# Kernel optimization log

Hardware: AMD Instinct MI355X
Metric: run time of the kernel (lower is better)

Reference implementation:

```python
import jax, jax.numpy as jnp
import numpy as np

NUM_HEADS = 8
IN_CH = 512
SCALING = float(IN_CH // 8) ** (-0.5)  # 0.125, as in the torch module


def _conv1x1(x, w, b):
    # x: [B,C,H,W], w: [O,C], b: [O]  (1x1 conv == channel matmul)
    return jnp.einsum('bchw,oc->bohw', x, w) + b[None, :, None, None]


def setup_inputs() -> dict:
    key = jax.random.key(0)
    ks = jax.random.split(key, 9)
    B, C, H, W = 4, IN_CH, 96, 96
    q = jax.random.normal(ks[0], (B, C, H, W), jnp.float32)
    v = jax.random.normal(ks[1], (B, C, H, W), jnp.float32)
    # xavier_uniform for [C,C] 1x1 conv weights
    limit = float(np.sqrt(6.0 / (C + C)))
    Wq = jax.random.uniform(ks[2], (C, C), jnp.float32, -limit, limit)
    Wk = jax.random.uniform(ks[3], (C, C), jnp.float32, -limit, limit)
    Wv = jax.random.uniform(ks[4], (C, C), jnp.float32, -limit, limit)
    bq = jnp.zeros((C,), jnp.float32)
    bk = jnp.zeros((C,), jnp.float32)
    bv = jnp.zeros((C,), jnp.float32)
    # gamma is init to 0 in the module; use a nonzero value so the output is nontrivial
    gamma = jax.random.normal(ks[5], (1,), jnp.float32) * 0.1
    return {'q': q, 'v': v, 'Wq': Wq, 'bq': bq, 'Wk': Wk, 'bk': bk,
            'Wv': Wv, 'bv': bv, 'gamma': gamma}


def reference(q, v, Wq, bq, Wk, bk, Wv, bv, gamma):
    B, C, H, W = q.shape
    nh = NUM_HEADS
    hd = C // nh
    t = _conv1x1(q, Wq, bq) * SCALING           # proj_query
    f = _conv1x1(q, Wk, bk)                     # proj_key
    g = _conv1x1(v, Wv, bv)                     # proj_value
    t = t.reshape(B * nh, hd, H, W)
    f = f.reshape(B * nh, hd, H, W)
    g = g.reshape(B * nh, hd, H, W)
    # criss-cross affinity: row (same y, all x') and column (same x, all y'!=y)
    e_row = jnp.einsum('bdyx,bdyi->byxi', t, f)  # [Bh, H, W, W]
    e_col = jnp.einsum('bdyx,bdix->byxi', t, f)  # [Bh, H, W, H]
    # exclude the current position from the column branch (CUDA kernel skips i==y)
    diag = (jnp.arange(H)[:, None, None] == jnp.arange(H)[None, None, :])  # [H,1,H]
    e_col = jnp.where(diag, -jnp.inf, e_col)
    attn = jax.nn.softmax(jnp.concatenate([e_row, e_col], axis=-1), axis=-1)  # [Bh,H,W,W+H]
    a_row, a_col = attn[..., :W], attn[..., W:]
    out = (jnp.einsum('byxi,bdyi->bdyx', a_row, g)
           + jnp.einsum('byxi,bdix->bdyx', a_col, g))  # [Bh, hd, H, W]
    out = out.reshape(B, C, H, W)
    return gamma[0] * out + v
```

## Files before the change

### kernel.cpp

```cpp
#include <hip/hip_runtime.h>
#include <hip/hip_bf16.h>

typedef __bf16 bf16;
typedef __attribute__((ext_vector_type(8))) __bf16 bf16x8;
typedef __attribute__((ext_vector_type(4))) float floatx4;

#define B_  4
#define C_  512
#define H_  96
#define W_  96
#define HD_ 64
#define HW_ 9216
#define BH_ 32
#define SCALING_ 0.125f
#define BHS_ 589824

static constexpr size_t T_ELEMS = (size_t)BH_ * HD_ * HW_;
static constexpr size_t S_ELEMS = (size_t)BH_ * HW_;

__global__ __launch_bounds__(256) void cast_w(
    const float* __restrict__ Wq, const float* __restrict__ Wk, const float* __restrict__ Wv,
    bf16* __restrict__ Wb)
{
    const int i  = blockIdx.x * 256 + threadIdx.x;
    const int e0 = i * 4;
    const int arr = e0 >> 18;
    const int off = e0 & 262143;
    const float* W = (arr == 0) ? Wq : (arr == 1) ? Wk : Wv;
    const float4 val = *(const float4*)(W + off);
    bf16 tmp[4] __attribute__((aligned(8)));
    tmp[0] = (bf16)val.x; tmp[1] = (bf16)val.y; tmp[2] = (bf16)val.z; tmp[3] = (bf16)val.w;
    *(uint2*)(Wb + e0) = *(const uint2*)tmp;
}

__global__ __launch_bounds__(256) void cast_qv(
    const float* __restrict__ q, const float* __restrict__ v,
    bf16* __restrict__ qbT, bf16* __restrict__ vbT)
{
    const int z = blockIdx.z;
    const int s = z >> 2, b = z & 3;
    const float* sb = (s ? v : q) + (size_t)b * C_ * HW_;
    bf16*       db = (s ? vbT : qbT) + (size_t)b * HW_ * C_;
    const int p0 = blockIdx.x * 64, c0 = blockIdx.y * 64;

    __shared__ float ts[64][65];
    const int tid = threadIdx.x;

    for (int i = tid; i < 1024; i += 256) {
        const int row = i >> 4, seg = i & 15;
        const float4 val = *(const float4*)(sb + (size_t)(c0 + row) * HW_ + p0 + seg * 4);
        ts[row][seg * 4 + 0] = val.x; ts[row][seg * 4 + 1] = val.y;
        ts[row][seg * 4 + 2] = val.z; ts[row][seg * 4 + 3] = val.w;
    }
    __syncthreads();
    for (int i = tid; i < 512; i += 256) {
        const int prow = i >> 3, cseg = i & 7;
        bf16 tmp[8] __attribute__((aligned(16)));
        #pragma unroll
        for (int k = 0; k < 8; k++) tmp[k] = (bf16)ts[cseg * 8 + k][prow];
        *(uint4*)(db + (size_t)(p0 + prow) * C_ + c0 + cseg * 8) = *(const uint4*)tmp;
    }
}

__device__ __forceinline__ void stage_swz(
    const bf16* __restrict__ A, const bf16* __restrict__ Bsrc,
    int o0, int p0, int k0, int tid, bf16* As, bf16* Bs)
{
    #pragma unroll
    for (int c = tid; c < 512; c += 256) {
        const int sc = c ^ ((c >> 3) & 7);
        const int row = sc >> 2, seg = sc & 3;
        const bf16* gA = A    + (size_t)(o0 + row) * C_ + k0 + seg * 8;
        const bf16* gB = Bsrc + (size_t)(p0 + row) * C_ + k0 + seg * 8;
#if __has_builtin(__builtin_amdgcn_global_load_lds)
        char* lA = (char*)As + (size_t)(c & ~63) * 16;
        char* lB = (char*)Bs + (size_t)(c & ~63) * 16;
        __builtin_amdgcn_global_load_lds((const __attribute__((address_space(1))) void*)gA,
                                         (__attribute__((address_space(3))) void*)lA, 16, 0, 0);
        __builtin_amdgcn_global_load_lds((const __attribute__((address_space(1))) void*)gB,
                                         (__attribute__((address_space(3))) void*)lB, 16, 0, 0);
#else
        *(uint4*)((char*)As + (size_t)c * 16) = *(const uint4*)gA;
        *(uint4*)((char*)Bs + (size_t)c * 16) = *(const uint4*)gB;
#endif
    }
}

__device__ __forceinline__ int swz_chunk(int r, int quad)
{
    return (r * 4 + quad) ^ ((r >> 1) & 7);
}

__device__ __forceinline__ void compute_swz(
    const bf16* As, const bf16* Bs,
    int mrow, int ncol, int l16, int quad, floatx4 acc[4][4])
{
    bf16x8 af[4], bf_[4];
    #pragma unroll
    for (int i = 0; i < 4; i++)
        af[i] = *(const bf16x8*)&As[swz_chunk(mrow + i * 16 + l16, quad) * 8];
    #pragma unroll
    for (int j = 0; j < 4; j++)
        bf_[j] = *(const bf16x8*)&Bs[swz_chunk(ncol + j * 16 + l16, quad) * 8];
    #pragma unroll
    for (int i = 0; i < 4; i++)
        #pragma unroll
        for (int j = 0; j < 4; j++)
            acc[i][j] = __builtin_amdgcn_mfma_f32_16x16x32_bf16(af[i], bf_[j], acc[i][j], 0, 0, 0);
}

__global__ __launch_bounds__(256) void conv_mfma(
    const bf16* __restrict__ Wb,
    const float* __restrict__ bq, const float* __restrict__ bk, const float* __restrict__ bv,
    const bf16* __restrict__ qbT, const bf16* __restrict__ vbT,
    bf16* __restrict__ tR, bf16* __restrict__ fR, bf16* __restrict__ g)
{
    const int z = blockIdx.z, arr = z >> 2, b = z & 3;
    const bf16* A    = Wb + (size_t)arr * C_ * C_;
    const bf16* Bsrc = ((arr == 2) ? vbT : qbT) + (size_t)b * HW_ * C_;
    const float* bias = (arr == 0) ? bq : (arr == 1) ? bk : bv;
    const float scale = (arr == 0) ? SCALING_ : 1.0f;

    const int p0 = blockIdx.x * 128;
    const int o0 = blockIdx.y * 128;

    __shared__ __align__(16) bf16 smem[17408];
    bf16* const As0 = smem;
    bf16* const Bs0 = smem + 4096;
    bf16* const As1 = smem + 8192;
    bf16* const Bs1 = smem + 12288;

    const int tid = threadIdx.x, lane = tid & 63;
    const int wave = tid >> 6, l16 = lane & 15, quad = lane >> 4;
    const int mrow = (wave >> 1) * 64, ncol = (wave & 1) * 64;

    floatx4 acc[4][4] = {};

    stage_swz(A, Bsrc, o0, p0, 0, tid, As0, Bs0);
    __syncthreads();

    for (int k0 = 0; k0 < C_; k0 += 64) {
        if (k0 + 32 < C_) stage_swz(A, Bsrc, o0, p0, k0 + 32, tid, As1, Bs1);
        compute_swz(As0, Bs0, mrow, ncol, l16, quad, acc);
        __syncthreads();
        if (k0 + 64 < C_) stage_swz(A, Bsrc, o0, p0, k0 + 64, tid, As0, Bs0);
        compute_swz(As1, Bs1, mrow, ncol, l16, quad, acc);
        __syncthreads();
    }

    if (arr < 2) {
        #pragma unroll
        for (int i = 0; i < 4; i++)
            #pragma unroll
            for (int r = 0; r < 4; r++) {
                const int ol_ = mrow + i * 16 + quad * 4 + r;
                const float bi = bias[o0 + ol_];
                #pragma unroll
                for (int j = 0; j < 4; j++) {
                    const int pl = ncol + j * 16 + l16;
                    smem[pl * 128 + (ol_ ^ ((pl & 7) << 3))] = (bf16)((acc[i][j][r] + bi) * scale);
                }
            }
        __syncthreads();
        bf16* dst = (arr == 0) ? tR : fR;
        #pragma unroll
        for (int c = tid; c < 2048; c += 256) {
            const int pl = c >> 4, oo = c & 15;
            const int pg = p0 + pl;
            const int y = pg / 96, x = pg - y * 96;
            const int og = o0 + oo * 8;
            const int bh = b * 8 + (og >> 6), d = og & 63;
            const size_t di = (size_t)bh * BHS_ + (size_t)y * 6144 + x * 64 + d;
            *(uint4*)(dst + di) = *(const uint4*)&smem[pl * 128 + ((oo ^ (pl & 7)) * 8)];
        }
    } else {
        const int TS = 136;
        #pragma unroll
        for (int i = 0; i < 4; i++)
            #pragma unroll
            for (int r = 0; r < 4; r++) {
                const int ol_ = mrow + i * 16 + quad * 4 + r;
                const float bi = bias[o0 + ol_];
                #pragma unroll
                for (int j = 0; j < 4; j++) {
                    const int pl = ncol + j * 16 + l16;
                    smem[ol_ * TS + pl] = (bf16)(acc[i][j][r] + bi);
                }
            }
        __syncthreads();
        #pragma unroll
        for (int c = tid; c < 2048; c += 256) {
            const int ol_ = c >> 4, po = c & 15;
            const size_t di = (size_t)(b * 512 + o0 + ol_) * HW_ + p0 + po * 8;
            *(uint4*)(g + di) = *(const uint4*)&smem[ol_ * TS + po * 8];
        }
    }
}

__global__ __launch_bounds__(256) void transpose_g(const bf16* __restrict__ src, bf16* __restrict__ dst)
{
    const int plane = blockIdx.y;
    const int y0 = blockIdx.x * 32;
    const bf16* s = src + (size_t)plane * HW_;
    bf16*       d = dst + (size_t)plane * HW_;

    __shared__ bf16 ts[32][100];
    const int tid = threadIdx.x;

    #pragma unroll
    for (int i = tid; i < 768; i += 256) {
        const int row = i / 24, seg = i % 24;
        *(uint2*)&ts[row][seg * 4] = *(const uint2*)(s + (size_t)(y0 + row) * W_ + seg * 4);
    }
    __syncthreads();
    #pragma unroll
    for (int i = tid; i < 768; i += 256) {
        const int x = i >> 3, yseg = i & 7;
        bf16 tmp[4] __attribute__((aligned(8)));
        #pragma unroll
        for (int k = 0; k < 4; k++) tmp[k] = ts[yseg * 4 + k][x];
        *(uint2*)(d + (size_t)x * H_ + y0 + yseg * 4) = *(const uint2*)tmp;
    }
}

__global__ __launch_bounds__(512) void attn_col(
    const bf16* __restrict__ tR, const bf16* __restrict__ fR, const bf16* __restrict__ gT,
    bf16* __restrict__ outC, float* __restrict__ mc, float* __restrict__ lc)
{
    const int x = blockIdx.x;
    const int bh = blockIdx.y;

    __shared__ __align__(16) bf16 tl[96][72];
    __shared__ __align__(16) bf16 fl[96][72];
    __shared__ __align__(16) bf16 el[96][104];

    const int tid = threadIdx.x;
    const size_t sbase = (size_t)bh * BHS_;

    for (int i = tid; i < 768; i += 512) {
        const int y = i >> 3, oct = i & 7;
        const size_t gi = sbase + (size_t)y * 6144 + (size_t)x * 64 + oct * 8;
        *(uint4*)&tl[y][oct * 8] = *(const uint4*)(tR + gi);
        *(uint4*)&fl[y][oct * 8] = *(const uint4*)(fR + gi);
    }
    __syncthreads();

    const int lane = tid & 63, wave = tid >> 6;
    const int l16 = lane & 15, quad = lane >> 4;

    __builtin_amdgcn_s_setprio(1);
    #pragma unroll
    for (int it = 0; it < 5; it++) {
        const int idx = wave + it * 8;
        if (idx < 36) {
            const int mt = idx / 6, nt = idx % 6;
            floatx4 a = {};
            #pragma unroll
            for (int ks = 0; ks < 2; ks++) {
                bf16x8 af = *(const bf16x8*)&tl[mt * 16 + l16][ks * 32 + quad * 8];
                bf16x8 bf_ = *(const bf16x8*)&fl[nt * 16 + l16][ks * 32 + quad * 8];
                a = __builtin_amdgcn_mfma_f32_16x16x32_bf16(af, bf_, a, 0, 0, 0);
            }
            #pragma unroll
            for (int r = 0; r < 4; r++) {
                const int row = mt * 16 + quad * 4 + r, col = nt * 16 + l16;
                el[row][col] = (row == col) ? (bf16)(-1e30f) : (bf16)a[r];
            }
        }
    }
    __builtin_amdgcn_s_setprio(0);
    __syncthreads();

    bf16 (*gl)[104] = (bf16 (*)[104])fl;
    const size_t gbase = sbase + (size_t)x * 96;
    for (int i = tid; i < 768; i += 512) {
        const int d = i / 12, seg = i % 12;
        *(uint4*)&gl[d][seg * 8] = *(const uint4*)(gT + gbase + (size_t)d * HW_ + seg * 8);
    }

    if (tid < 384) {
        const int r = tid >> 2, qu = tid & 3;
        float vals[24];
        float m = -1e30f;
        #pragma unroll
        for (int k = 0; k < 3; k++) {
            bf16x8 v8 = *(const bf16x8*)&el[r][qu * 24 + k * 8];
            #pragma unroll
            for (int e = 0; e < 8; e++) { vals[k * 8 + e] = (float)v8[e]; m = fmaxf(m, vals[k * 8 + e]); }
        }
        m = fmaxf(m, __shfl_xor(m, 1));
        m = fmaxf(m, __shfl_xor(m, 2));
        float s = 0.f;
        #pragma unroll
        for (int k = 0; k < 3; k++) {
            bf16 tmp[8] __attribute__((aligned(16)));
            #pragma unroll
            for (int e = 0; e < 8; e++) {
                const float p = __expf(vals[k * 8 + e] - m);
                s += p; tmp[e] = (bf16)p;
            }
            *(uint4*)&el[r][qu * 24 + k * 8] = *(const uint4*)tmp;
        }
        s += __shfl_xor(s, 1);
        s += __shfl_xor(s, 2);
        if (qu == 0) {
            mc[(size_t)bh * HW_ + x * 96 + r] = m;
            lc[(size_t)bh * HW_ + x * 96 + r] = s;
        }
    }
    __syncthreads();

    bf16 (*ol)[72] = tl;
    __builtin_amdgcn_s_setprio(1);
    #pragma unroll
    for (int it = 0; it < 3; it++) {
        const int idx = wave + it * 8;
        const int mt = idx >> 2, nt = idx & 3;
        floatx4 a = {};
        #pragma unroll
        for (int ks = 0; ks < 3; ks++) {
            bf16x8 pf = *(const bf16x8*)&el[mt * 16 + l16][ks * 32 + quad * 8];
            bf16x8 gf = *(const bf16x8*)&gl[nt * 16 + l16][ks * 32 + quad * 8];
            a = __builtin_amdgcn_mfma_f32_16x16x32_bf16(pf, gf, a, 0, 0, 0);
        }
        #pragma unroll
        for (int r = 0; r < 4; r++)
            ol[mt * 16 + quad * 4 + r][nt * 16 + l16] = (bf16)a[r];
    }
    __builtin_amdgcn_s_setprio(0);
    __syncthreads();

    bf16* ob = outC + sbase + (size_t)x * 6144;
    for (int i = tid; i < 768; i += 512) {
        const int j = i >> 3, oct = i & 7;
        *(uint4*)(ob + (size_t)j * 64 + oct * 8) = *(const uint4*)&ol[j][oct * 8];
    }
}

__global__ __launch_bounds__(512) void attn_row_merge(
    const bf16* __restrict__ tR, const bf16* __restrict__ fR, const bf16* __restrict__ g,
    const bf16* __restrict__ outC, const float* __restrict__ mc, const float* __restrict__ lc,
    const float* __restrict__ v, const float* __restrict__ gamma, float* __restrict__ out)
{
    const int y = blockIdx.x;
    const int bh = blockIdx.y;

    __shared__ __align__(16) bf16 tl[96][72];
    __shared__ __align__(16) bf16 fl[96][72];
    __shared__ __align__(16) bf16 el[96][104];
    __shared__ float mll[96], lll[96], wrl[96], wcl[96];

    const int tid = threadIdx.x;
    const size_t sbase = (size_t)bh * BHS_;
    const size_t slice = sbase + (size_t)y * 6144;

    for (int i = tid; i < 768; i += 512) {
        const int j = i >> 3, oct = i & 7;
        *(uint4*)&tl[j][oct * 8] = *(const uint4*)(tR + slice + (size_t)j * 64 + oct * 8);
        *(uint4*)&fl[j][oct * 8] = *(const uint4*)(fR + slice + (size_t)j * 64 + oct * 8);
    }

    uint4 oc0, oc1 = {};
    {
        const int xx = tid >> 3, oct = tid & 7;
        oc0 = *(const uint4*)(outC + sbase + (size_t)xx * 6144 + (size_t)y * 64 + oct * 8);
    }
    if (tid < 256) {
        const int i1 = tid + 512, xx = i1 >> 3, oct = i1 & 7;
        oc1 = *(const uint4*)(outC + sbase + (size_t)xx * 6144 + (size_t)y * 64 + oct * 8);
    }
    float4 vp0a, vp0b, vp1a = {}, vp1b = {};
    {
        const int xo = tid >> 6, d = tid & 63;
        const size_t ob = sbase + (size_t)d * HW_ + (size_t)y * 96 + xo * 8;
        vp0a = *(const float4*)(v + ob);
        vp0b = *(const float4*)(v + ob + 4);
    }
    if (tid < 256) {
        const int i1 = tid + 512, xo = i1 >> 6, d = i1 & 63;
        const size_t ob = sbase + (size_t)d * HW_ + (size_t)y * 96 + xo * 8;
        vp1a = *(const float4*)(v + ob);
        vp1b = *(const float4*)(v + ob + 4);
    }
    float mcv = 0.f, lcv = 0.f;
    if (tid < 96) {
        mcv = mc[(size_t)bh * HW_ + tid * 96 + y];
        lcv = lc[(size_t)bh * HW_ + tid * 96 + y];
    }
    __syncthreads();

    const int lane = tid & 63, wave = tid >> 6;
    const int l16 = lane & 15, quad = lane >> 4;

    __builtin_amdgcn_s_setprio(1);
    #pragma unroll
    for (int it = 0; it < 5; it++) {
        const int idx = wave + it * 8;
        if (idx < 36) {
            const int mt = idx / 6, nt = idx % 6;
            floatx4 a = {};
            #pragma unroll
            for (int ks = 0; ks < 2; ks++) {
                bf16x8 af = *(const bf16x8*)&tl[mt * 16 + l16][ks * 32 + quad * 8];
                bf16x8 bf_ = *(const bf16x8*)&fl[nt * 16 + l16][ks * 32 + quad * 8];
                a = __builtin_amdgcn_mfma_f32_16x16x32_bf16(af, bf_, a, 0, 0, 0);
            }
            #pragma unroll
            for (int r = 0; r < 4; r++)
                el[mt * 16 + quad * 4 + r][nt * 16 + l16] = (bf16)a[r];
        }
    }
    __builtin_amdgcn_s_setprio(0);
    __syncthreads();

    bf16 (*gl)[104] = (bf16 (*)[104])tl;
    const size_t gbase = sbase + (size_t)y * 96;
    for (int i = tid; i < 768; i += 512) {
        const int d = i / 12, seg = i % 12;
        *(uint4*)&gl[d][seg * 8] = *(const uint4*)(g + gbase + (size_t)d * HW_ + seg * 8);
    }

    bf16 (*ocl)[72] = fl;
    {
        const int xx = tid >> 3, oct = tid & 7;
        *(uint4*)&ocl[xx][oct * 8] = oc0;
    }
    if (tid < 256) {
        const int i1 = tid + 512, xx = i1 >> 3, oct = i1 & 7;
        *(uint4*)&ocl[xx][oct * 8] = oc1;
    }

    if (tid < 384) {
        const int r = tid >> 2, qu = tid & 3;
        float vals[24];
        float m = -1e30f;
        #pragma unroll
        for (int k = 0; k < 3; k++) {
            bf16x8 v8 = *(const bf16x8*)&el[r][qu * 24 + k * 8];
            #pragma unroll
            for (int e = 0; e < 8; e++) { vals[k * 8 + e] = (float)v8[e]; m = fmaxf(m, vals[k * 8 + e]); }
        }
        m = fmaxf(m, __shfl_xor(m, 1));
        m = fmaxf(m, __shfl_xor(m, 2));
        float s = 0.f;
        #pragma unroll
        for (int k = 0; k < 3; k++) {
            bf16 tmp[8] __attribute__((aligned(16)));
            #pragma unroll
            for (int e = 0; e < 8; e++) {
                const float p = __expf(vals[k * 8 + e] - m);
                s += p; tmp[e] = (bf16)p;
            }
            *(uint4*)&el[r][qu * 24 + k * 8] = *(const uint4*)tmp;
        }
        s += __shfl_xor(s, 1);
        s += __shfl_xor(s, 2);
        if (qu == 0) { mll[r] = m; lll[r] = s; }
    }
    __syncthreads();

    if (tid < 96) {
        const float mrv = mll[tid], lrv = lll[tid];
        const float mm = fmaxf(mrv, mcv);
        const float wr = __expf(mrv - mm), wc = __expf(mcv - mm);
        const float dn = lrv * wr + lcv * wc;
        wrl[tid] = wr / dn;
        wcl[tid] = wc / dn;
    }
    floatx4 pa[3] = {};
    __builtin_amdgcn_s_setprio(1);
    #pragma unroll
    for (int it = 0; it < 3; it++) {
        const int idx = wave + it * 8;
        const int mt = idx >> 2, nt = idx & 3;
        #pragma unroll
        for (int ks = 0; ks < 3; ks++) {
            bf16x8 pf = *(const bf16x8*)&el[mt * 16 + l16][ks * 32 + quad * 8];
            bf16x8 gf = *(const bf16x8*)&gl[nt * 16 + l16][ks * 32 + quad * 8];
            pa[it] = __builtin_amdgcn_mfma_f32_16x16x32_bf16(pf, gf, pa[it], 0, 0, 0);
        }
    }
    __builtin_amdgcn_s_setprio(0);
    __syncthreads();

    #pragma unroll
    for (int it = 0; it < 3; it++) {
        const int idx = wave + it * 8;
        const int mt = idx >> 2, nt = idx & 3;
        #pragma unroll
        for (int r = 0; r < 4; r++)
            el[mt * 16 + quad * 4 + r][nt * 16 + l16] = (bf16)pa[it][r];
    }
    __syncthreads();

    const float gam = gamma[0];
    {
        const int xo = tid >> 6, d = tid & 63;
        const int x0 = xo * 8;
        float res[8];
        #pragma unroll
        for (int k = 0; k < 8; k++) {
            const int xx = x0 + k;
            res[k] = (float)el[xx][d] * wrl[xx] + (float)ocl[xx][d] * wcl[xx];
        }
        const size_t ob = sbase + (size_t)d * HW_ + (size_t)y * 96 + x0;
        float4 r0, r1;
        r0.x = gam * res[0] + vp0a.x; r0.y = gam * res[1] + vp0a.y;
        r0.z = gam * res[2] + vp0a.z; r0.w = gam * res[3] + vp0a.w;
        r1.x = gam * res[4] + vp0b.x; r1.y = gam * res[5] + vp0b.y;
        r1.z = gam * res[6] + vp0b.z; r1.w = gam * res[7] + vp0b.w;
        *(float4*)(out + ob) = r0;
        *(float4*)(out + ob + 4) = r1;
    }
    if (tid < 256) {
        const int i1 = tid + 512;
        const int xo = i1 >> 6, d = i1 & 63;
        const int x0 = xo * 8;
        float res[8];
        #pragma unroll
        for (int k = 0; k < 8; k++) {
            const int xx = x0 + k;
            res[k] = (float)el[xx][d] * wrl[xx] + (float)ocl[xx][d] * wcl[xx];
        }
        const size_t ob = sbase + (size_t)d * HW_ + (size_t)y * 96 + x0;
        float4 r0, r1;
        r0.x = gam * res[0] + vp1a.x; r0.y = gam * res[1] + vp1a.y;
        r0.z = gam * res[2] + vp1a.z; r0.w = gam * res[3] + vp1a.w;
        r1.x = gam * res[4] + vp1b.x; r1.y = gam * res[5] + vp1b.y;
        r1.z = gam * res[6] + vp1b.z; r1.w = gam * res[7] + vp1b.w;
        *(float4*)(out + ob) = r0;
        *(float4*)(out + ob + 4) = r1;
    }
}

extern "C" void kernel_launch(void* const* d_in, const int* in_sizes, int n_in,
                              void* d_out, int out_size, void* d_ws, size_t ws_size,
                              hipStream_t stream)
{
    const float* q     = (const float*)d_in[0];
    const float* v     = (const float*)d_in[1];
    const float* Wq    = (const float*)d_in[2];
    const float* bq    = (const float*)d_in[3];
    const float* Wk    = (const float*)d_in[4];
    const float* bk    = (const float*)d_in[5];
    const float* Wv    = (const float*)d_in[6];
    const float* bv    = (const float*)d_in[7];
    const float* gamma = (const float*)d_in[8];
    float* out = (float*)d_out;

    char* w = (char*)d_ws;
    const size_t Tb = T_ELEMS * sizeof(bf16);
    bf16* qbT  = (bf16*)(w + 0 * Tb);
    bf16* vbT  = (bf16*)(w + 1 * Tb);
    bf16* tR   = (bf16*)(w + 2 * Tb);
    bf16* fR   = (bf16*)(w + 3 * Tb);
    bf16* g    = (bf16*)(w + 4 * Tb);
    bf16* gT   = (bf16*)(w + 1 * Tb);
    bf16* outC = (bf16*)(w + 0 * Tb);
    bf16* Wb   = (bf16*)(w + 6 * Tb);
    float* mc  = (float*)(w + 6 * Tb + 1572864);
    float* lc  = mc + S_ELEMS;

    cast_w  <<<dim3(768), 256, 0, stream>>>(Wq, Wk, Wv, Wb);
    cast_qv <<<dim3(144, 8, 8), 256, 0, stream>>>(q, v, qbT, vbT);
    conv_mfma<<<dim3(72, 4, 12), 256, 0, stream>>>(Wb, bq, bk, bv, qbT, vbT, tR, fR, g);
    transpose_g<<<dim3(3, 2048), 256, 0, stream>>>(g, gT);
    attn_col<<<dim3(96, BH_), 512, 0, stream>>>(tR, fR, gT, outC, mc, lc);
    attn_row_merge<<<dim3(96, BH_), 512, 0, stream>>>(tR, fR, g, outC, mc, lc, v, gamma, out);
}
```

Measured before the change: 400.0 us.

## Triple-buffer conv GEMM with one barrier per step and fuse weight cast

The 1x1-conv MFMA GEMM moves from a double-buffered loop with two __syncthreads per 64-wide k step to a three-stage shared-memory ring. Each 32-wide k step now uses explicit vmcnt waits and a single s_barrier, which lets global loads run two stages ahead of compute. The separate weight-cast kernel is folded into cast_qv as an extra z-slice, saving one launch. The trade-offs are more LDS per block (48KB instead of 34KB) and reliance on hand-tuned vmcnt counts, which must match the number of loads stage_swz issues.

New measurement: 390.5 us. 2.4% less time.

```diff
diff --git a/kernel.cpp b/kernel.cpp
--- a/kernel.cpp
+++ b/kernel.cpp
@@ -18,33 +18,37 @@
 static constexpr size_t T_ELEMS = (size_t)BH_ * HD_ * HW_;
 static constexpr size_t S_ELEMS = (size_t)BH_ * HW_;
 
-__global__ __launch_bounds__(256) void cast_w(
-    const float* __restrict__ Wq, const float* __restrict__ Wk, const float* __restrict__ Wv,
-    bf16* __restrict__ Wb)
-{
-    const int i  = blockIdx.x * 256 + threadIdx.x;
-    const int e0 = i * 4;
-    const int arr = e0 >> 18;
-    const int off = e0 & 262143;
-    const float* W = (arr == 0) ? Wq : (arr == 1) ? Wk : Wv;
-    const float4 val = *(const float4*)(W + off);
-    bf16 tmp[4] __attribute__((aligned(8)));
-    tmp[0] = (bf16)val.x; tmp[1] = (bf16)val.y; tmp[2] = (bf16)val.z; tmp[3] = (bf16)val.w;
-    *(uint2*)(Wb + e0) = *(const uint2*)tmp;
-}
-
 __global__ __launch_bounds__(256) void cast_qv(
     const float* __restrict__ q, const float* __restrict__ v,
-    bf16* __restrict__ qbT, bf16* __restrict__ vbT)
+    const float* __restrict__ Wq, const float* __restrict__ Wk, const float* __restrict__ Wv,
+    bf16* __restrict__ qbT, bf16* __restrict__ vbT, bf16* __restrict__ Wb)
 {
     const int z = blockIdx.z;
+    const int tid = threadIdx.x;
+
+    if (z == 8) {
+        const int bi = blockIdx.y * 144 + blockIdx.x;
+        if (bi < 768) {
+            const int i  = bi * 256 + tid;
+            const int e0 = i * 4;
+            const int arr = e0 >> 18;
+            const int off = e0 & 262143;
+            const float* W = (arr == 0) ? Wq : (arr == 1) ? Wk : Wv;
+            const float4 val = *(const float4*)(W + off);
+            bf16 tmp[4] __attribute__((aligned(8)));
+            tmp[0] = (bf16)val.x; tmp[1] = (bf16)val.y;
+            tmp[2] = (bf16)val.z; tmp[3] = (bf16)val.w;
+            *(uint2*)(Wb + e0) = *(const uint2*)tmp;
+        }
+        return;
+    }
+
     const int s = z >> 2, b = z & 3;
     const float* sb = (s ? v : q) + (size_t)b * C_ * HW_;
     bf16*       db = (s ? vbT : qbT) + (size_t)b * HW_ * C_;
     const int p0 = blockIdx.x * 64, c0 = blockIdx.y * 64;
 
     __shared__ float ts[64][65];
-    const int tid = threadIdx.x;
 
     for (int i = tid; i < 1024; i += 256) {
         const int row = i >> 4, seg = i & 15;
@@ -124,11 +128,7 @@
     const int p0 = blockIdx.x * 128;
     const int o0 = blockIdx.y * 128;
 
-    __shared__ __align__(16) bf16 smem[17408];
-    bf16* const As0 = smem;
-    bf16* const Bs0 = smem + 4096;
-    bf16* const As1 = smem + 8192;
-    bf16* const Bs1 = smem + 12288;
+    __shared__ __align__(16) bf16 smem[24576];
 
     const int tid = threadIdx.x, lane = tid & 63;
     const int wave = tid >> 6, l16 = lane & 15, quad = lane >> 4;
@@ -136,17 +136,24 @@
 
     floatx4 acc[4][4] = {};
 
-    stage_swz(A, Bsrc, o0, p0, 0, tid, As0, Bs0);
-    __syncthreads();
-
-    for (int k0 = 0; k0 < C_; k0 += 64) {
-        if (k0 + 32 < C_) stage_swz(A, Bsrc, o0, p0, k0 + 32, tid, As1, Bs1);
-        compute_swz(As0, Bs0, mrow, ncol, l16, quad, acc);
-        __syncthreads();
-        if (k0 + 64 < C_) stage_swz(A, Bsrc, o0, p0, k0 + 64, tid, As0, Bs0);
-        compute_swz(As1, Bs1, mrow, ncol, l16, quad, acc);
-        __syncthreads();
-    }
+    stage_swz(A, Bsrc, o0, p0, 0,  tid, smem,        smem + 4096);
+    stage_swz(A, Bsrc, o0, p0, 32, tid, smem + 8192, smem + 12288);
+
+    #pragma unroll
+    for (int i = 0; i < 16; i++) {
+        if (i == 15) asm volatile("s_waitcnt vmcnt(0)" ::: "memory");
+        else         asm volatile("s_waitcnt vmcnt(4)" ::: "memory");
+        __builtin_amdgcn_sched_barrier(0);
+        __builtin_amdgcn_s_barrier();
+        __builtin_amdgcn_sched_barrier(0);
+        if (i + 2 < 16) {
+            bf16* base = smem + ((i + 2) % 3) * 8192;
+            stage_swz(A, Bsrc, o0, p0, (i + 2) * 32, tid, base, base + 4096);
+        }
+        const bf16* cur = smem + (i % 3) * 8192;
+        compute_swz(cur, cur + 4096, mrow, ncol, l16, quad, acc);
+    }
+    __syncthreads();
 
     if (arr < 2) {
         #pragma unroll
@@ -561,8 +568,7 @@
     float* mc  = (float*)(w + 6 * Tb + 1572864);
     float* lc  = mc + S_ELEMS;
 
-    cast_w  <<<dim3(768), 256, 0, stream>>>(Wq, Wk, Wv, Wb);
-    cast_qv <<<dim3(144, 8, 8), 256, 0, stream>>>(q, v, qbT, vbT);
+    cast_qv <<<dim3(144, 8, 9), 256, 0, stream>>>(q, v, Wq, Wk, Wv, qbT, vbT, Wb);
     conv_mfma<<<dim3(72, 4, 12), 256, 0, stream>>>(Wb, bq, bk, bv, qbT, vbT, tR, fR, g);
     transpose_g<<<dim3(3, 2048), 256, 0, stream>>>(g, gT);
     attn_col<<<dim3(96, BH_), 512, 0, stream>>>(tR, fR, gT, outC, mc, lc);
```
